# Performance work log

Measured on AMD Instinct MI355X. Metric: run time of the kernel, lower is better.

## Reference

```python
import math
import jax, jax.numpy as jnp
import numpy as np
from jax import lax

# FPN anchor layout: 1024x768 image, strides {4,8,16,32,64}, 3 anchors/location
NUM_PER_LEVEL = (147456, 36864, 9216, 2304, 576)
A_TOTAL = sum(NUM_PER_LEVEL)
BATCH = 8
PRE_NMS_TOP_N = 1000   # testing
POST_NMS_TOP_N = 1000  # testing
NMS_THRESH = 0.7
SCORE_THRESH = 0.0
MIN_SIZE = 1.0
IMG_H, IMG_W = 768.0, 1024.0
BBOX_XFORM_CLIP = math.log(1000.0 / 16.0)


def setup_inputs() -> dict:
    key = jax.random.key(0)
    k1, k2, k3, k4, k5, k6 = jax.random.split(key, 6)
    objectness = jax.random.normal(k1, (BATCH, A_TOTAL), jnp.float32)
    pred_bbox_deltas = jax.random.normal(k2, (BATCH, A_TOTAL, 4), jnp.float32) * 0.2
    # valid anchor boxes (x1, y1, x2, y2)
    cx = jax.random.uniform(k3, (A_TOTAL,), jnp.float32) * IMG_W
    cy = jax.random.uniform(k4, (A_TOTAL,), jnp.float32) * IMG_H
    w = 16.0 + jax.random.uniform(k5, (A_TOTAL,), jnp.float32) * 176.0
    h = 16.0 + jax.random.uniform(k6, (A_TOTAL,), jnp.float32) * 176.0
    anchors = jnp.stack([cx - 0.5 * w, cy - 0.5 * h, cx + 0.5 * w, cy + 0.5 * h], -1)
    return {"objectness": objectness, "pred_bbox_deltas": pred_bbox_deltas, "anchors": anchors}


def _nms_image(boxes, scores, lvl, valid):
    """batched_nms (level-offset trick) + post-NMS top-k, fixed shapes.
    boxes [K,4], scores [K], lvl [K] int, valid [K] bool -> [POST_NMS_TOP_N, 5]"""
    K = boxes.shape[0]
    s = jnp.where(valid, scores, -1.0)
    order = jnp.argsort(-s)  # decreasing score (invalid last)
    b = boxes[order]
    s = s[order]
    v = valid[order]
    # offset boxes per level so cross-level boxes never overlap (torchvision batched_nms)
    offset = lvl[order].astype(b.dtype) * (jnp.max(lax.stop_gradient(boxes)) + 1.0)
    nb = lax.stop_gradient(b) + offset[:, None]
    area = (nb[:, 2] - nb[:, 0]) * (nb[:, 3] - nb[:, 1])
    lt = jnp.maximum(nb[:, None, :2], nb[None, :, :2])  # [K,K,2]
    rb = jnp.minimum(nb[:, None, 2:], nb[None, :, 2:])
    wh = jnp.clip(rb - lt, 0.0)
    inter = wh[..., 0] * wh[..., 1]
    iou = inter / jnp.maximum(area[:, None] + area[None, :] - inter, 1e-9)
    pos = jnp.arange(K)

    def body(keep, i):
        sup = keep[i] & (iou[i] > NMS_THRESH) & (pos > i)
        return keep & ~sup, None

    keep, _ = lax.scan(body, v, pos)
    masked = jnp.where(keep, s, -1.0)
    top_s, top_i = lax.top_k(masked, POST_NMS_TOP_N)  # kept, decreasing score
    sel_b = b[top_i]
    ok = top_s > -0.5
    sel_b = jnp.where(ok[:, None], sel_b, 0.0)
    top_s = jnp.where(ok, top_s, 0.0)
    return jnp.concatenate([sel_b, top_s[:, None]], axis=-1)


def reference(objectness, pred_bbox_deltas, anchors):
    # --- box decode (BoxCoder, weights (1,1,1,1)) ---
    wa = anchors[:, 2] - anchors[:, 0]
    ha = anchors[:, 3] - anchors[:, 1]
    cxa = anchors[:, 0] + 0.5 * wa
    cya = anchors[:, 1] + 0.5 * ha
    dx, dy = pred_bbox_deltas[..., 0], pred_bbox_deltas[..., 1]
    dw = jnp.minimum(pred_bbox_deltas[..., 2], BBOX_XFORM_CLIP)
    dh = jnp.minimum(pred_bbox_deltas[..., 3], BBOX_XFORM_CLIP)
    pcx = dx * wa + cxa
    pcy = dy * ha + cya
    pw = jnp.exp(dw) * wa
    ph = jnp.exp(dh) * ha
    proposals = jnp.stack(
        [pcx - 0.5 * pw, pcy - 0.5 * ph, pcx + 0.5 * pw, pcy + 0.5 * ph], axis=-1
    )  # [B, A, 4]

    # --- per-level pre-NMS top-k (_get_top_n_idx) ---
    levels = jnp.concatenate(
        [jnp.full((n,), i, jnp.int32) for i, n in enumerate(NUM_PER_LEVEL)]
    )
    idx_parts = []
    off = 0
    for n in NUM_PER_LEVEL:
        k = min(PRE_NMS_TOP_N, n)
        _, ti = lax.top_k(objectness[:, off:off + n], k)
        idx_parts.append(ti + off)
        off += n
    top_idx = jnp.concatenate(idx_parts, axis=1)  # [B, K]

    scores = jax.nn.sigmoid(jnp.take_along_axis(objectness, top_idx, axis=1))
    lvl = levels[top_idx]
    boxes = jnp.take_along_axis(proposals, top_idx[..., None], axis=1)  # [B,K,4]

    # --- clip to image ---
    x1 = jnp.clip(boxes[..., 0], 0.0, IMG_W)
    y1 = jnp.clip(boxes[..., 1], 0.0, IMG_H)
    x2 = jnp.clip(boxes[..., 2], 0.0, IMG_W)
    y2 = jnp.clip(boxes[..., 3], 0.0, IMG_H)
    boxes = jnp.stack([x1, y1, x2, y2], axis=-1)

    # remove_small_boxes + score threshold (as validity mask; fixed shapes)
    valid = ((x2 - x1) >= MIN_SIZE) & ((y2 - y1) >= MIN_SIZE) & (scores >= SCORE_THRESH)

    # --- per-image batched NMS + post-NMS top-k ---
    return jax.vmap(_nms_image)(boxes, scores, lvl, valid)  # [B, POST_NMS_TOP_N, 5]
```

## Files before the change

### kernel.cpp

```cpp
#include <hip/hip_runtime.h>
#include <math.h>

#pragma clang fp contract(off)

#define A_TOTAL 196416
#define BATCH 8
#define KTOT 4576
#define NLEV 5
#define MSPLIT 16
#define RCAP 6144

static __device__ const int d_aoff[NLEV] = {0, 147456, 184320, 193536, 195840};
static __device__ const int d_n[NLEV]    = {147456, 36864, 9216, 2304, 576};
static __device__ const int d_k[NLEV]    = {1000, 1000, 1000, 1000, 576};
static __device__ const int d_spl[NLEV]  = {8, 2, 1, 1, 1};
static __device__ const int d_bp[NLEV]   = {0, 8, 10, 11, 12};
static __device__ const int d_pb_l[13]    = {0,0,0,0,0,0,0,0,1,1,2,3,4};
static __device__ const int d_pb_part[13] = {0,1,2,3,4,5,6,7,0,1,0,0,0};

#define TM_IOU (0.699999988079071044921875 + 0x1p-25)

__device__ inline unsigned int mono(float f) {
  unsigned int u = __float_as_uint(f);
  return (u & 0x80000000u) ? ~u : (u | 0x80000000u);
}
__device__ inline float imono(unsigned int m) {
  return __uint_as_float((m & 0x80000000u) ? (m & 0x7FFFFFFFu) : ~m);
}

__device__ inline int cnt_gt(const float* A, int n, float s) {
  int lo = 0, hi = n;
  while (lo < hi) { int mid = (lo + hi) >> 1; if (A[mid] > s) lo = mid + 1; else hi = mid; }
  return lo;
}
__device__ inline int cnt_ge(const float* A, int n, float s) {
  int lo = 0, hi = n;
  while (lo < hi) { int mid = (lo + hi) >> 1; if (A[mid] >= s) lo = mid + 1; else hi = mid; }
  return lo;
}

__global__ __launch_bounds__(1024) void k_hist(const float* __restrict__ obj,
                                               int* __restrict__ hist_g,
                                               int* __restrict__ cnt_g,
                                               float* __restrict__ maxblk) {
  int blk = blockIdx.x;
  int tid = threadIdx.x;
  if (blk == 0) {
    for (int i = tid; i < 640; i += 1024) maxblk[i] = 0.0f;
    for (int i = tid; i < 40; i += 1024) cnt_g[i] = 0;
  }
  int b = blk / 13, pb = blk % 13;
  int l = d_pb_l[pb], part = d_pb_part[pb];
  int slice = d_n[l] / d_spl[l];
  int start = d_aoff[l] + part * slice;
  const float4* p4 = (const float4*)(obj + (size_t)b * A_TOTAL + start);
  int s4 = slice >> 2;
  __shared__ int h[4096];
  for (int i = tid; i < 4096; i += 1024) h[i] = 0;
  __syncthreads();
  for (int i = tid; i < s4; i += 1024) {
    float4 v = p4[i];
    atomicAdd(&h[mono(v.x) >> 20], 1);
    atomicAdd(&h[mono(v.y) >> 20], 1);
    atomicAdd(&h[mono(v.z) >> 20], 1);
    atomicAdd(&h[mono(v.w) >> 20], 1);
  }
  __syncthreads();
  int* outp = hist_g + (size_t)blk * 4096;
  for (int i = tid; i < 4096; i += 1024) outp[i] = h[i];
}

__global__ __launch_bounds__(1024) void k_collect(const float* __restrict__ obj,
                                                  const int* __restrict__ hist_g,
                                                  int* __restrict__ cnt_g,
                                                  unsigned long long* __restrict__ cand_g) {
  int blk = blockIdx.x;
  int b = blk / 13, pb = blk % 13;
  int l = d_pb_l[pb], part = d_pb_part[pb];
  int bl = b * NLEV + l;
  const int k = d_k[l];
  int tid = threadIdx.x;
  __shared__ int t[4096];
  __shared__ int grp[256];
  __shared__ unsigned int sP;
  __shared__ __align__(16) unsigned long long lbuf[RCAP];
  __shared__ int s_cnt, s_base;
  int parts = d_spl[l];
  const int* hb = hist_g + (size_t)(b * 13 + d_bp[l]) * 4096;
  for (int bin = tid; bin < 4096; bin += 1024) {
    int s = 0;
    for (int p = 0; p < parts; ++p) s += hb[p * 4096 + bin];
    t[bin] = s;
  }
  if (tid == 0) s_cnt = 0;
  __syncthreads();
  if (tid < 256) {
    int s = 0;
    for (int j = 0; j < 16; ++j) s += t[tid * 16 + j];
    grp[tid] = s;
  }
  __syncthreads();
  if (tid == 0) {
    int cum = 0, g, d;
    for (g = 255; g >= 0; --g) {
      if (cum + grp[g] >= k) break;
      cum += grp[g];
    }
    for (d = 15; d >= 0; --d) {
      int c = t[g * 16 + d];
      if (cum + c >= k) break;
      cum += c;
    }
    sP = (unsigned int)(g * 16 + d);
  }
  __syncthreads();
  unsigned int P = sP;
  int slice = d_n[l] / parts;
  int start = d_aoff[l] + part * slice;
  const float4* p4 = (const float4*)(obj + (size_t)b * A_TOTAL + start);
  int s4 = slice >> 2;
  int lbase = part * slice;
  for (int i = tid; i < s4; i += 1024) {
    float4 v = p4[i];
    unsigned int a[4] = {mono(v.x), mono(v.y), mono(v.z), mono(v.w)};
#pragma unroll
    for (int c = 0; c < 4; ++c) {
      if ((a[c] >> 20) >= P) {
        int slot = atomicAdd(&s_cnt, 1);
        if (slot < RCAP) {
          int idx = lbase + 4 * i + c;
          lbuf[slot] = ((unsigned long long)a[c] << 32) |
                       (unsigned int)(~(unsigned int)idx);
        }
      }
    }
  }
  __syncthreads();
  int cnt = min(s_cnt, RCAP);
  if (tid == 0) s_base = atomicAdd(&cnt_g[bl], cnt);
  __syncthreads();
  int base = s_base;
  for (int i = tid; i < cnt; i += 1024) {
    int slot = base + i;
    if (slot < RCAP) cand_g[(size_t)bl * RCAP + slot] = lbuf[i];
  }
}

__global__ __launch_bounds__(256) void k_rankdec(const unsigned long long* __restrict__ cand_g,
                                                 const int* __restrict__ cnt_g,
                                                 const float* __restrict__ deltas,
                                                 const float* __restrict__ anchors,
                                                 float* __restrict__ sc0,
                                                 float4* __restrict__ box0,
                                                 float* __restrict__ maxblk) {
  int bl = blockIdx.x >> 4, part = blockIdx.x & 15;
  int b = bl / NLEV, l = bl % NLEV;
  const int k = d_k[l], aoff = d_aoff[l];
  int cnt = min(cnt_g[bl], RCAP);
  if (part * 256 >= cnt) return;
  __shared__ __align__(16) unsigned long long cb[RCAP];
  __shared__ unsigned int s_max;
  int tid = threadIdx.x;
  if (tid == 0) s_max = 0u;
  const unsigned long long* src = cand_g + (size_t)bl * RCAP;
  for (int i = tid; i < cnt; i += 256) cb[i] = src[i];
  __syncthreads();
  int myi = part * 256 + tid;
  float mx = 0.0f;
  if (myi < cnt) {
    unsigned long long e = cb[myi];
    int rank = 0;
    int nc2 = cnt >> 1;
    const ulonglong2* c2 = (const ulonglong2*)cb;
    for (int j = 0; j < nc2; ++j) {
      ulonglong2 v = c2[j];
      rank += (v.x > e) + (v.y > e);
    }
    if (cnt & 1) rank += (cb[cnt - 1] > e);
    if (rank < k) {
      unsigned int k32 = (unsigned int)(e >> 32);
      unsigned int idx = ~(unsigned int)(e & 0xFFFFFFFFull);
      float o = imono(k32);
      int gidx = aoff + (int)idx;
      const float* dl = deltas + ((size_t)b * A_TOTAL + gidx) * 4;
      const float* an = anchors + (size_t)gidx * 4;
      float a0 = an[0], a1 = an[1], a2 = an[2], a3 = an[3];
      float wa = a2 - a0, ha = a3 - a1;
      float cxa = a0 + 0.5f * wa, cya = a1 + 0.5f * ha;
      float dx = dl[0], dy = dl[1];
      const float CLIPV = 4.135166556742356f;
      float dw = fminf(dl[2], CLIPV), dh = fminf(dl[3], CLIPV);
      float pcx = dx * wa + cxa;
      float pcy = dy * ha + cya;
      float pw = (float)exp((double)dw) * wa;
      float ph = (float)exp((double)dh) * ha;
      float x1 = pcx - 0.5f * pw, y1 = pcy - 0.5f * ph;
      float x2 = pcx + 0.5f * pw, y2 = pcy + 0.5f * ph;
      x1 = fminf(fmaxf(x1, 0.0f), 1024.0f);
      x2 = fminf(fmaxf(x2, 0.0f), 1024.0f);
      y1 = fminf(fmaxf(y1, 0.0f), 768.0f);
      y2 = fminf(fmaxf(y2, 0.0f), 768.0f);
      float s = (float)(1.0 / (1.0 + exp(-(double)o)));
      bool valid = ((x2 - x1) >= 1.0f) && ((y2 - y1) >= 1.0f) && (s >= 0.0f);
      sc0[bl * 1024 + rank] = valid ? s : -1.0f;
      box0[bl * 1024 + rank] = make_float4(x1, y1, x2, y2);
      mx = fmaxf(fmaxf(x1, y1), fmaxf(x2, y2));
    }
  }
#pragma unroll
  for (int s = 1; s < 64; s <<= 1) mx = fmaxf(mx, __shfl_xor(mx, s));
  if ((tid & 63) == 0) atomicMax(&s_max, __float_as_uint(mx));
  __syncthreads();
  if (tid == 0) maxblk[blockIdx.x] = __uint_as_float(s_max);
}

__global__ __launch_bounds__(1024) void k_mask(const float* __restrict__ sc0,
                                               const float4* __restrict__ box0,
                                               const float* __restrict__ maxblk,
                                               float* __restrict__ lvlsc,
                                               float4* __restrict__ lvlraw,
                                               int* __restrict__ g_V,
                                               unsigned long long* __restrict__ masks) {
  int blk = blockIdx.x;
  int bl = blk / MSPLIT, part = blk % MSPLIT;
  int b = bl / NLEV, l = bl % NLEV;
  const int k = d_k[l];
  int tid = threadIdx.x, lane = tid & 63, w = tid >> 6;
  __shared__ float4 lbox[1024];
  __shared__ float s_mv;
  __shared__ int s_wcnt[16];
  if (w == 0) {
    float v = (lane < 80) ? maxblk[b * 80 + lane] : 0.0f;
    float v2 = (lane + 64 < 80) ? maxblk[b * 80 + lane + 64] : 0.0f;
    v = fmaxf(v, v2);
#pragma unroll
    for (int s = 1; s < 64; s <<= 1) v = fmaxf(v, __shfl_xor(v, s));
    if (lane == 0) s_mv = v;
  }
  bool in = tid < k;
  float s = in ? sc0[bl * 1024 + tid] : -1.0f;
  bool valid = in && (s >= 0.0f);
  unsigned long long mb = __ballot(valid);
  if (lane == 0) s_wcnt[w] = __popcll(mb);
  __syncthreads();
  int pre = 0;
  for (int ww = 0; ww < w; ++ww) pre += s_wcnt[ww];
  int j = pre + __popcll(mb & ((1ull << lane) - 1ull));
  int V = 0;
  for (int ww = 0; ww < 16; ++ww) V += s_wcnt[ww];
  float off = (float)l * (s_mv + 1.0f);
  if (valid) {
    float4 bx = box0[bl * 1024 + tid];
    lbox[j] = make_float4(bx.x + off, bx.y + off, bx.z + off, bx.w + off);
    if (part == 0) {
      lvlsc[bl * 1024 + j] = s;
      lvlraw[bl * 1024 + j] = bx;
    }
  }
  if (part == 0 && tid == 0) g_V[bl] = V;
  __syncthreads();
  int row0 = part * 64;
  if (row0 >= V) return;
  int i = row0 + lane;
  if (i >= V) return;
  float4 bb = lbox[i];
  float ba = (bb.z - bb.x) * (bb.w - bb.y);
  unsigned long long bits = 0ull;
  int jbase = w * 64;
  if (jbase + 63 > i && jbase < V) {
    int jhi = min(64, V - jbase);
    for (int jo = 0; jo < jhi; ++jo) {
      int jj = jbase + jo;
      float4 cb = lbox[jj];
      float ca = (cb.z - cb.x) * (cb.w - cb.y);
      float xx1 = fmaxf(bb.x, cb.x), yy1 = fmaxf(bb.y, cb.y);
      float xx2 = fminf(bb.z, cb.z), yy2 = fminf(bb.w, cb.w);
      float wd = fmaxf(xx2 - xx1, 0.0f), ht = fmaxf(yy2 - yy1, 0.0f);
      float inter = wd * ht;
      float denom = fmaxf(ba + ca - inter, 1e-9f);
      if ((jj > i) && ((double)inter >= TM_IOU * (double)denom)) bits |= (1ull << jo);
    }
  }
  masks[((size_t)bl * 16 + w) * 1024 + i] = bits;
}

__global__ __launch_bounds__(1024) void k_scan(const unsigned long long* __restrict__ masks,
                                               const int* __restrict__ g_V,
                                               unsigned long long* __restrict__ keepbits) {
  int bl = blockIdx.x;
  int tid = threadIdx.x, lane = tid & 63, w = tid >> 6;
  int V = g_V[bl];
  const int nch = (V + 63) / 64;
  const unsigned long long* M = masks + (size_t)bl * 16 * 1024;
  __shared__ unsigned long long s_remv[16];
  __shared__ unsigned long long s_D[2][72];
  __shared__ unsigned long long s_dw;
  if (tid < 16) s_remv[tid] = ~0ull;
  int base_w = w * 64;
  unsigned long long init_w;
  if (V <= base_w) init_w = ~0ull;
  else if (V >= base_w + 64) init_w = 0ull;
  else init_w = (~0ull) << (V - base_w);
  if (w == 0 && nch > 0) s_D[0][lane] = (lane < V) ? M[lane] : 0ull;
  if (tid < 8) { s_D[0][64 + tid] = 0ull; s_D[1][64 + tid] = 0ull; }
  unsigned long long acc = 0ull;
  __syncthreads();

  for (int c = 0; c < nch; ++c) {
    unsigned long long val = 0ull;
    int r = 64 * c + lane;
    if (w > c && w < nch && r < V) val = M[(size_t)w * 1024 + r];
    if (w == c) {
      unsigned long long red = acc;
#pragma unroll
      for (int s = 1; s < 64; s <<= 1) red |= __shfl_xor(red, s);
      unsigned long long dw = init_w | red;
      const unsigned long long* D = s_D[c & 1];
      unsigned long long pb[8];
#pragma unroll
      for (int u = 0; u < 8; ++u) pb[u] = D[u];
#pragma unroll
      for (int g = 0; g < 8; ++g) {
#pragma unroll
        for (int u = 0; u < 8; ++u) {
          int jj = g * 8 + u;
          if (!((dw >> jj) & 1ull)) dw |= pb[u];
          pb[u] = D[jj + 8];
        }
      }
      if (lane == 0) { s_dw = dw; s_remv[c] = dw; }
    }
    if (w == c + 1 && w < nch) {
      int rr = 64 * (c + 1) + lane;
      s_D[(c + 1) & 1][lane] = (rr < V) ? M[(size_t)(c + 1) * 1024 + rr] : 0ull;
    }
    __syncthreads();
    if (w > c && w < nch) {
      unsigned long long kept = ~s_dw;
      if ((kept >> lane) & 1ull) acc |= val;
    }
    __syncthreads();
  }
  if (tid < 16) keepbits[bl * 16 + tid] = ~s_remv[tid];
}

__global__ __launch_bounds__(1024) void k_out(const float* __restrict__ lvlsc,
                                              const float4* __restrict__ lvlraw,
                                              const unsigned long long* __restrict__ keepbits,
                                              const int* __restrict__ g_V,
                                              float* __restrict__ out) {
  int b = blockIdx.x;
  int tid = threadIdx.x, lane = tid & 63, wv = tid >> 6;
  __shared__ float ksc[NLEV * 1024];
  __shared__ int kj[NLEV * 1024];
  __shared__ int sK[NLEV];
  __shared__ int s_wcnt[16];
  for (int i = tid; i < 5000; i += 1024) out[(size_t)b * 5000 + i] = 0.0f;
  for (int l = 0; l < NLEV; ++l) {
    int bl = b * NLEV + l;
    int V = g_V[bl];
    bool kept = (tid < V) && ((keepbits[bl * 16 + (tid >> 6)] >> (tid & 63)) & 1ull);
    unsigned long long mb = __ballot(kept);
    if (lane == 0) s_wcnt[wv] = __popcll(mb);
    __syncthreads();
    int pre = 0;
    for (int w = 0; w < wv; ++w) pre += s_wcnt[w];
    int r = pre + __popcll(mb & ((1ull << lane) - 1ull));
    if (kept) { ksc[l * 1024 + r] = lvlsc[bl * 1024 + tid]; kj[l * 1024 + r] = tid; }
    if (tid == 0) {
      int t = 0;
      for (int w = 0; w < 16; ++w) t += s_wcnt[w];
      sK[l] = t;
    }
    __syncthreads();
  }
  int K[NLEV];
  for (int l = 0; l < NLEV; ++l) K[l] = sK[l];
  for (int l = 0; l < NLEV; ++l) {
    if (tid < K[l]) {
      float s = ksc[l * 1024 + tid];
      int rank = tid;
      for (int l2 = 0; l2 < NLEV; ++l2) {
        if (l2 == l) continue;
        const float* A = ksc + l2 * 1024;
        rank += (l2 < l) ? cnt_ge(A, K[l2], s) : cnt_gt(A, K[l2], s);
      }
      if (rank < 1000) {
        float4 bx = lvlraw[(size_t)(b * NLEV + l) * 1024 + kj[l * 1024 + tid]];
        float* op = out + (size_t)b * 5000 + (size_t)rank * 5;
        op[0] = bx.x; op[1] = bx.y; op[2] = bx.z; op[3] = bx.w; op[4] = s;
      }
    }
  }
}

extern "C" void kernel_launch(void* const* d_in, const int* in_sizes, int n_in,
                              void* d_out, int out_size, void* d_ws, size_t ws_size,
                              hipStream_t stream) {
  const float* obj     = (const float*)d_in[0];
  const float* deltas  = (const float*)d_in[1];
  const float* anchors = (const float*)d_in[2];
  float* out = (float*)d_out;

  char* p = (char*)d_ws;
  float4* box0   = (float4*)p; p += (size_t)40 * 1024 * sizeof(float4);
  float4* lvlraw = (float4*)p; p += (size_t)40 * 1024 * sizeof(float4);
  unsigned long long* cand_g   = (unsigned long long*)p; p += (size_t)40 * RCAP * 8;
  unsigned long long* masks    = (unsigned long long*)p; p += (size_t)40 * 16 * 1024 * 8;
  unsigned long long* keepbits = (unsigned long long*)p; p += (size_t)40 * 16 * 8;
  int*   hist_g = (int*)p;   p += (size_t)104 * 4096 * 4;
  int*   cnt_g  = (int*)p;   p += 40 * 4;
  float* maxblk = (float*)p; p += 640 * 4;
  float* sc0    = (float*)p; p += (size_t)40 * 1024 * 4;
  float* lvlsc  = (float*)p; p += (size_t)40 * 1024 * 4;
  int*   g_V    = (int*)p;   p += 40 * 4;

  hipLaunchKernelGGL(k_hist, dim3(BATCH * 13), dim3(1024), 0, stream,
                     obj, hist_g, cnt_g, maxblk);
  hipLaunchKernelGGL(k_collect, dim3(BATCH * 13), dim3(1024), 0, stream,
                     obj, hist_g, cnt_g, cand_g);
  hipLaunchKernelGGL(k_rankdec, dim3(BATCH * NLEV * 16), dim3(256), 0, stream,
                     cand_g, cnt_g, deltas, anchors, sc0, box0, maxblk);
  hipLaunchKernelGGL(k_mask, dim3(BATCH * NLEV * MSPLIT), dim3(1024), 0, stream,
                     sc0, box0, maxblk, lvlsc, lvlraw, g_V, masks);
  hipLaunchKernelGGL(k_scan, dim3(BATCH * NLEV), dim3(1024), 0, stream,
                     masks, g_V, keepbits);
  hipLaunchKernelGGL(k_out, dim3(BATCH), dim3(1024), 0, stream,
                     lvlsc, lvlraw, keepbits, g_V, out);
}
```

Before: 208.9 us.

## Fuse six NMS pipeline kernels into one cooperative kernel with grid syncs

Replaces the six separate kernel launches (histogram, collect, rank/decode, mask, scan, output) with a single cooperative kernel of 256 blocks that separates the stages with grid-wide barriers. Shared memory is pooled into one buffer reused by each stage. The rank/decode stage now uses 1024-thread tasks and reads candidates straight from global memory instead of staging them in shared memory. This removes per-launch overhead and inter-kernel gaps, but every stage is now limited to 256 resident blocks, grid.sync has its own cost, and the large shared-memory footprint may constrain occupancy.

```diff
diff --git a/kernel.cpp b/kernel.cpp
--- a/kernel.cpp
+++ b/kernel.cpp
@@ -1,14 +1,19 @@
 #include <hip/hip_runtime.h>
+#include <hip/hip_cooperative_groups.h>
 #include <math.h>
 
 #pragma clang fp contract(off)
+
+namespace cg = cooperative_groups;
+typedef unsigned long long u64;
+typedef unsigned int u32;
 
 #define A_TOTAL 196416
 #define BATCH 8
-#define KTOT 4576
 #define NLEV 5
 #define MSPLIT 16
 #define RCAP 6144
+#define NP3 (RCAP / 1024)
 
 static __device__ const int d_aoff[NLEV] = {0, 147456, 184320, 193536, 195840};
 static __device__ const int d_n[NLEV]    = {147456, 36864, 9216, 2304, 576};
@@ -20,14 +25,13 @@
 
 #define TM_IOU (0.699999988079071044921875 + 0x1p-25)
 
-__device__ inline unsigned int mono(float f) {
-  unsigned int u = __float_as_uint(f);
+__device__ inline u32 mono(float f) {
+  u32 u = __float_as_uint(f);
   return (u & 0x80000000u) ? ~u : (u | 0x80000000u);
 }
-__device__ inline float imono(unsigned int m) {
+__device__ inline float imono(u32 m) {
   return __uint_as_float((m & 0x80000000u) ? (m & 0x7FFFFFFFu) : ~m);
 }
-
 __device__ inline int cnt_gt(const float* A, int n, float s) {
   int lo = 0, hi = n;
   while (lo < hi) { int mid = (lo + hi) >> 1; if (A[mid] > s) lo = mid + 1; else hi = mid; }
@@ -39,356 +43,340 @@
   return lo;
 }
 
-__global__ __launch_bounds__(1024) void k_hist(const float* __restrict__ obj,
-                                               int* __restrict__ hist_g,
-                                               int* __restrict__ cnt_g,
-                                               float* __restrict__ maxblk) {
-  int blk = blockIdx.x;
-  int tid = threadIdx.x;
+__global__ __launch_bounds__(1024) void k_fused(
+    const float* __restrict__ obj, const float* __restrict__ deltas,
+    const float* __restrict__ anchors, float* __restrict__ out,
+    int* __restrict__ hist_g, int* __restrict__ cnt_g,
+    float* __restrict__ maxblk, u64* __restrict__ cand_g,
+    float* __restrict__ sc0, float4* __restrict__ box0,
+    float* __restrict__ lvlsc, float4* __restrict__ lvlraw,
+    int* __restrict__ g_V, u64* __restrict__ masks,
+    u64* __restrict__ keepbits) {
+  cg::grid_group grid = cg::this_grid();
+  int blk = blockIdx.x, tid = threadIdx.x, lane = tid & 63, w = tid >> 6;
+
+  __shared__ __align__(16) unsigned char smem[66560];
+  __shared__ int s_wcnt[16];
+  __shared__ int s_cnt, s_base;
+  __shared__ u32 sP, s_max;
+  __shared__ float s_mv;
+  __shared__ int sK[NLEV];
+  __shared__ u64 s_remv[16];
+  __shared__ u64 s_D[2][72];
+  __shared__ u64 s_dw;
+
   if (blk == 0) {
-    for (int i = tid; i < 640; i += 1024) maxblk[i] = 0.0f;
+    for (int i = tid; i < 240; i += 1024) maxblk[i] = 0.0f;
     for (int i = tid; i < 40; i += 1024) cnt_g[i] = 0;
   }
-  int b = blk / 13, pb = blk % 13;
-  int l = d_pb_l[pb], part = d_pb_part[pb];
-  int slice = d_n[l] / d_spl[l];
-  int start = d_aoff[l] + part * slice;
-  const float4* p4 = (const float4*)(obj + (size_t)b * A_TOTAL + start);
-  int s4 = slice >> 2;
-  __shared__ int h[4096];
-  for (int i = tid; i < 4096; i += 1024) h[i] = 0;
-  __syncthreads();
-  for (int i = tid; i < s4; i += 1024) {
-    float4 v = p4[i];
-    atomicAdd(&h[mono(v.x) >> 20], 1);
-    atomicAdd(&h[mono(v.y) >> 20], 1);
-    atomicAdd(&h[mono(v.z) >> 20], 1);
-    atomicAdd(&h[mono(v.w) >> 20], 1);
-  }
-  __syncthreads();
-  int* outp = hist_g + (size_t)blk * 4096;
-  for (int i = tid; i < 4096; i += 1024) outp[i] = h[i];
-}
-
-__global__ __launch_bounds__(1024) void k_collect(const float* __restrict__ obj,
-                                                  const int* __restrict__ hist_g,
-                                                  int* __restrict__ cnt_g,
-                                                  unsigned long long* __restrict__ cand_g) {
-  int blk = blockIdx.x;
-  int b = blk / 13, pb = blk % 13;
-  int l = d_pb_l[pb], part = d_pb_part[pb];
-  int bl = b * NLEV + l;
-  const int k = d_k[l];
-  int tid = threadIdx.x;
-  __shared__ int t[4096];
-  __shared__ int grp[256];
-  __shared__ unsigned int sP;
-  __shared__ __align__(16) unsigned long long lbuf[RCAP];
-  __shared__ int s_cnt, s_base;
-  int parts = d_spl[l];
-  const int* hb = hist_g + (size_t)(b * 13 + d_bp[l]) * 4096;
-  for (int bin = tid; bin < 4096; bin += 1024) {
-    int s = 0;
-    for (int p = 0; p < parts; ++p) s += hb[p * 4096 + bin];
-    t[bin] = s;
-  }
-  if (tid == 0) s_cnt = 0;
-  __syncthreads();
-  if (tid < 256) {
-    int s = 0;
-    for (int j = 0; j < 16; ++j) s += t[tid * 16 + j];
-    grp[tid] = s;
-  }
-  __syncthreads();
-  if (tid == 0) {
-    int cum = 0, g, d;
-    for (g = 255; g >= 0; --g) {
-      if (cum + grp[g] >= k) break;
-      cum += grp[g];
-    }
-    for (d = 15; d >= 0; --d) {
-      int c = t[g * 16 + d];
-      if (cum + c >= k) break;
-      cum += c;
-    }
-    sP = (unsigned int)(g * 16 + d);
-  }
-  __syncthreads();
-  unsigned int P = sP;
-  int slice = d_n[l] / parts;
-  int start = d_aoff[l] + part * slice;
-  const float4* p4 = (const float4*)(obj + (size_t)b * A_TOTAL + start);
-  int s4 = slice >> 2;
-  int lbase = part * slice;
-  for (int i = tid; i < s4; i += 1024) {
-    float4 v = p4[i];
-    unsigned int a[4] = {mono(v.x), mono(v.y), mono(v.z), mono(v.w)};
-#pragma unroll
-    for (int c = 0; c < 4; ++c) {
-      if ((a[c] >> 20) >= P) {
-        int slot = atomicAdd(&s_cnt, 1);
-        if (slot < RCAP) {
-          int idx = lbase + 4 * i + c;
-          lbuf[slot] = ((unsigned long long)a[c] << 32) |
-                       (unsigned int)(~(unsigned int)idx);
+  if (blk < 104) {
+    int b = blk / 13, pb = blk % 13;
+    int l = d_pb_l[pb], part = d_pb_part[pb];
+    int slice = d_n[l] / d_spl[l];
+    int start = d_aoff[l] + part * slice;
+    const float4* p4 = (const float4*)(obj + (size_t)b * A_TOTAL + start);
+    int s4 = slice >> 2;
+    int* h = (int*)smem;
+    for (int i = tid; i < 4096; i += 1024) h[i] = 0;
+    __syncthreads();
+    for (int i = tid; i < s4; i += 1024) {
+      float4 v = p4[i];
+      atomicAdd(&h[mono(v.x) >> 20], 1);
+      atomicAdd(&h[mono(v.y) >> 20], 1);
+      atomicAdd(&h[mono(v.z) >> 20], 1);
+      atomicAdd(&h[mono(v.w) >> 20], 1);
+    }
+    __syncthreads();
+    int* outp = hist_g + (size_t)blk * 4096;
+    for (int i = tid; i < 4096; i += 1024) outp[i] = h[i];
+  }
+  grid.sync();
+
+  if (blk < 104) {
+    int b = blk / 13, pb = blk % 13;
+    int l = d_pb_l[pb], part = d_pb_part[pb];
+    int bl = b * NLEV + l;
+    const int k = d_k[l];
+    int* t = (int*)smem;
+    int* grp = (int*)(smem + 16384);
+    u64* lbuf = (u64*)(smem + 17408);
+    int parts = d_spl[l];
+    const int* hb = hist_g + (size_t)(b * 13 + d_bp[l]) * 4096;
+    for (int bin = tid; bin < 4096; bin += 1024) {
+      int s = 0;
+      for (int p = 0; p < parts; ++p) s += hb[p * 4096 + bin];
+      t[bin] = s;
+    }
+    if (tid == 0) s_cnt = 0;
+    __syncthreads();
+    if (tid < 256) {
+      int s = 0;
+      for (int j = 0; j < 16; ++j) s += t[tid * 16 + j];
+      grp[tid] = s;
+    }
+    __syncthreads();
+    if (tid == 0) {
+      int cum = 0, g, d;
+      for (g = 255; g >= 0; --g) {
+        if (cum + grp[g] >= k) break;
+        cum += grp[g];
+      }
+      for (d = 15; d >= 0; --d) {
+        int c = t[g * 16 + d];
+        if (cum + c >= k) break;
+        cum += c;
+      }
+      sP = (u32)(g * 16 + d);
+    }
+    __syncthreads();
+    u32 P = sP;
+    int slice = d_n[l] / parts;
+    int start = d_aoff[l] + part * slice;
+    const float4* p4 = (const float4*)(obj + (size_t)b * A_TOTAL + start);
+    int s4 = slice >> 2;
+    int lbase = part * slice;
+    for (int i = tid; i < s4; i += 1024) {
+      float4 v = p4[i];
+      u32 a[4] = {mono(v.x), mono(v.y), mono(v.z), mono(v.w)};
+#pragma unroll
+      for (int c = 0; c < 4; ++c) {
+        if ((a[c] >> 20) >= P) {
+          int slot = atomicAdd(&s_cnt, 1);
+          if (slot < RCAP) {
+            int idx = lbase + 4 * i + c;
+            lbuf[slot] = ((u64)a[c] << 32) | (u32)(~(u32)idx);
+          }
         }
       }
     }
-  }
-  __syncthreads();
-  int cnt = min(s_cnt, RCAP);
-  if (tid == 0) s_base = atomicAdd(&cnt_g[bl], cnt);
-  __syncthreads();
-  int base = s_base;
-  for (int i = tid; i < cnt; i += 1024) {
-    int slot = base + i;
-    if (slot < RCAP) cand_g[(size_t)bl * RCAP + slot] = lbuf[i];
-  }
-}
-
-__global__ __launch_bounds__(256) void k_rankdec(const unsigned long long* __restrict__ cand_g,
-                                                 const int* __restrict__ cnt_g,
-                                                 const float* __restrict__ deltas,
-                                                 const float* __restrict__ anchors,
-                                                 float* __restrict__ sc0,
-                                                 float4* __restrict__ box0,
-                                                 float* __restrict__ maxblk) {
-  int bl = blockIdx.x >> 4, part = blockIdx.x & 15;
-  int b = bl / NLEV, l = bl % NLEV;
-  const int k = d_k[l], aoff = d_aoff[l];
-  int cnt = min(cnt_g[bl], RCAP);
-  if (part * 256 >= cnt) return;
-  __shared__ __align__(16) unsigned long long cb[RCAP];
-  __shared__ unsigned int s_max;
-  int tid = threadIdx.x;
-  if (tid == 0) s_max = 0u;
-  const unsigned long long* src = cand_g + (size_t)bl * RCAP;
-  for (int i = tid; i < cnt; i += 256) cb[i] = src[i];
-  __syncthreads();
-  int myi = part * 256 + tid;
-  float mx = 0.0f;
-  if (myi < cnt) {
-    unsigned long long e = cb[myi];
-    int rank = 0;
-    int nc2 = cnt >> 1;
-    const ulonglong2* c2 = (const ulonglong2*)cb;
-    for (int j = 0; j < nc2; ++j) {
-      ulonglong2 v = c2[j];
-      rank += (v.x > e) + (v.y > e);
-    }
-    if (cnt & 1) rank += (cb[cnt - 1] > e);
-    if (rank < k) {
-      unsigned int k32 = (unsigned int)(e >> 32);
-      unsigned int idx = ~(unsigned int)(e & 0xFFFFFFFFull);
-      float o = imono(k32);
-      int gidx = aoff + (int)idx;
-      const float* dl = deltas + ((size_t)b * A_TOTAL + gidx) * 4;
-      const float* an = anchors + (size_t)gidx * 4;
-      float a0 = an[0], a1 = an[1], a2 = an[2], a3 = an[3];
-      float wa = a2 - a0, ha = a3 - a1;
-      float cxa = a0 + 0.5f * wa, cya = a1 + 0.5f * ha;
-      float dx = dl[0], dy = dl[1];
-      const float CLIPV = 4.135166556742356f;
-      float dw = fminf(dl[2], CLIPV), dh = fminf(dl[3], CLIPV);
-      float pcx = dx * wa + cxa;
-      float pcy = dy * ha + cya;
-      float pw = (float)exp((double)dw) * wa;
-      float ph = (float)exp((double)dh) * ha;
-      float x1 = pcx - 0.5f * pw, y1 = pcy - 0.5f * ph;
-      float x2 = pcx + 0.5f * pw, y2 = pcy + 0.5f * ph;
-      x1 = fminf(fmaxf(x1, 0.0f), 1024.0f);
-      x2 = fminf(fmaxf(x2, 0.0f), 1024.0f);
-      y1 = fminf(fmaxf(y1, 0.0f), 768.0f);
-      y2 = fminf(fmaxf(y2, 0.0f), 768.0f);
-      float s = (float)(1.0 / (1.0 + exp(-(double)o)));
-      bool valid = ((x2 - x1) >= 1.0f) && ((y2 - y1) >= 1.0f) && (s >= 0.0f);
-      sc0[bl * 1024 + rank] = valid ? s : -1.0f;
-      box0[bl * 1024 + rank] = make_float4(x1, y1, x2, y2);
-      mx = fmaxf(fmaxf(x1, y1), fmaxf(x2, y2));
-    }
-  }
-#pragma unroll
-  for (int s = 1; s < 64; s <<= 1) mx = fmaxf(mx, __shfl_xor(mx, s));
-  if ((tid & 63) == 0) atomicMax(&s_max, __float_as_uint(mx));
-  __syncthreads();
-  if (tid == 0) maxblk[blockIdx.x] = __uint_as_float(s_max);
-}
-
-__global__ __launch_bounds__(1024) void k_mask(const float* __restrict__ sc0,
-                                               const float4* __restrict__ box0,
-                                               const float* __restrict__ maxblk,
-                                               float* __restrict__ lvlsc,
-                                               float4* __restrict__ lvlraw,
-                                               int* __restrict__ g_V,
-                                               unsigned long long* __restrict__ masks) {
-  int blk = blockIdx.x;
-  int bl = blk / MSPLIT, part = blk % MSPLIT;
-  int b = bl / NLEV, l = bl % NLEV;
-  const int k = d_k[l];
-  int tid = threadIdx.x, lane = tid & 63, w = tid >> 6;
-  __shared__ float4 lbox[1024];
-  __shared__ float s_mv;
-  __shared__ int s_wcnt[16];
-  if (w == 0) {
-    float v = (lane < 80) ? maxblk[b * 80 + lane] : 0.0f;
-    float v2 = (lane + 64 < 80) ? maxblk[b * 80 + lane + 64] : 0.0f;
-    v = fmaxf(v, v2);
-#pragma unroll
-    for (int s = 1; s < 64; s <<= 1) v = fmaxf(v, __shfl_xor(v, s));
-    if (lane == 0) s_mv = v;
-  }
-  bool in = tid < k;
-  float s = in ? sc0[bl * 1024 + tid] : -1.0f;
-  bool valid = in && (s >= 0.0f);
-  unsigned long long mb = __ballot(valid);
-  if (lane == 0) s_wcnt[w] = __popcll(mb);
-  __syncthreads();
-  int pre = 0;
-  for (int ww = 0; ww < w; ++ww) pre += s_wcnt[ww];
-  int j = pre + __popcll(mb & ((1ull << lane) - 1ull));
-  int V = 0;
-  for (int ww = 0; ww < 16; ++ww) V += s_wcnt[ww];
-  float off = (float)l * (s_mv + 1.0f);
-  if (valid) {
-    float4 bx = box0[bl * 1024 + tid];
-    lbox[j] = make_float4(bx.x + off, bx.y + off, bx.z + off, bx.w + off);
-    if (part == 0) {
-      lvlsc[bl * 1024 + j] = s;
-      lvlraw[bl * 1024 + j] = bx;
-    }
-  }
-  if (part == 0 && tid == 0) g_V[bl] = V;
-  __syncthreads();
-  int row0 = part * 64;
-  if (row0 >= V) return;
-  int i = row0 + lane;
-  if (i >= V) return;
-  float4 bb = lbox[i];
-  float ba = (bb.z - bb.x) * (bb.w - bb.y);
-  unsigned long long bits = 0ull;
-  int jbase = w * 64;
-  if (jbase + 63 > i && jbase < V) {
-    int jhi = min(64, V - jbase);
-    for (int jo = 0; jo < jhi; ++jo) {
-      int jj = jbase + jo;
-      float4 cb = lbox[jj];
-      float ca = (cb.z - cb.x) * (cb.w - cb.y);
-      float xx1 = fmaxf(bb.x, cb.x), yy1 = fmaxf(bb.y, cb.y);
-      float xx2 = fminf(bb.z, cb.z), yy2 = fminf(bb.w, cb.w);
-      float wd = fmaxf(xx2 - xx1, 0.0f), ht = fmaxf(yy2 - yy1, 0.0f);
-      float inter = wd * ht;
-      float denom = fmaxf(ba + ca - inter, 1e-9f);
-      if ((jj > i) && ((double)inter >= TM_IOU * (double)denom)) bits |= (1ull << jo);
-    }
-  }
-  masks[((size_t)bl * 16 + w) * 1024 + i] = bits;
-}
-
-__global__ __launch_bounds__(1024) void k_scan(const unsigned long long* __restrict__ masks,
-                                               const int* __restrict__ g_V,
-                                               unsigned long long* __restrict__ keepbits) {
-  int bl = blockIdx.x;
-  int tid = threadIdx.x, lane = tid & 63, w = tid >> 6;
-  int V = g_V[bl];
-  const int nch = (V + 63) / 64;
-  const unsigned long long* M = masks + (size_t)bl * 16 * 1024;
-  __shared__ unsigned long long s_remv[16];
-  __shared__ unsigned long long s_D[2][72];
-  __shared__ unsigned long long s_dw;
-  if (tid < 16) s_remv[tid] = ~0ull;
-  int base_w = w * 64;
-  unsigned long long init_w;
-  if (V <= base_w) init_w = ~0ull;
-  else if (V >= base_w + 64) init_w = 0ull;
-  else init_w = (~0ull) << (V - base_w);
-  if (w == 0 && nch > 0) s_D[0][lane] = (lane < V) ? M[lane] : 0ull;
-  if (tid < 8) { s_D[0][64 + tid] = 0ull; s_D[1][64 + tid] = 0ull; }
-  unsigned long long acc = 0ull;
-  __syncthreads();
-
-  for (int c = 0; c < nch; ++c) {
-    unsigned long long val = 0ull;
-    int r = 64 * c + lane;
-    if (w > c && w < nch && r < V) val = M[(size_t)w * 1024 + r];
-    if (w == c) {
-      unsigned long long red = acc;
-#pragma unroll
-      for (int s = 1; s < 64; s <<= 1) red |= __shfl_xor(red, s);
-      unsigned long long dw = init_w | red;
-      const unsigned long long* D = s_D[c & 1];
-      unsigned long long pb[8];
-#pragma unroll
-      for (int u = 0; u < 8; ++u) pb[u] = D[u];
-#pragma unroll
-      for (int g = 0; g < 8; ++g) {
-#pragma unroll
-        for (int u = 0; u < 8; ++u) {
-          int jj = g * 8 + u;
-          if (!((dw >> jj) & 1ull)) dw |= pb[u];
-          pb[u] = D[jj + 8];
+    __syncthreads();
+    int cnt = min(s_cnt, RCAP);
+    if (tid == 0) s_base = atomicAdd(&cnt_g[bl], cnt);
+    __syncthreads();
+    int base = s_base;
+    for (int i = tid; i < cnt; i += 1024) {
+      int slot = base + i;
+      if (slot < RCAP) cand_g[(size_t)bl * RCAP + slot] = lbuf[i];
+    }
+  }
+  grid.sync();
+
+  for (int task = blk; task < 40 * NP3; task += 256) {
+    int bl = task / NP3, part = task % NP3;
+    int cnt = min(cnt_g[bl], RCAP);
+    if (part * 1024 >= cnt) continue;
+    int b = bl / NLEV, l = bl % NLEV;
+    const int k = d_k[l], aoff = d_aoff[l];
+    const u64* src = cand_g + (size_t)bl * RCAP;
+    if (tid == 0) s_max = 0u;
+    __syncthreads();
+    int myi = part * 1024 + tid;
+    float mx = 0.0f;
+    if (myi < cnt) {
+      u64 e = src[myi];
+      int rank = 0;
+      const ulonglong2* c2 = (const ulonglong2*)src;
+      int nc2 = cnt >> 1;
+#pragma unroll 4
+      for (int j = 0; j < nc2; ++j) {
+        ulonglong2 v = c2[j];
+        rank += (v.x > e) + (v.y > e);
+      }
+      if (cnt & 1) rank += (src[cnt - 1] > e);
+      if (rank < k) {
+        u32 k32 = (u32)(e >> 32);
+        u32 idx = ~(u32)(e & 0xFFFFFFFFull);
+        float o = imono(k32);
+        int gidx = aoff + (int)idx;
+        const float* dl = deltas + ((size_t)b * A_TOTAL + gidx) * 4;
+        const float* an = anchors + (size_t)gidx * 4;
+        float a0 = an[0], a1 = an[1], a2 = an[2], a3 = an[3];
+        float wa = a2 - a0, ha = a3 - a1;
+        float cxa = a0 + 0.5f * wa, cya = a1 + 0.5f * ha;
+        float dx = dl[0], dy = dl[1];
+        const float CLIPV = 4.135166556742356f;
+        float dw = fminf(dl[2], CLIPV), dh = fminf(dl[3], CLIPV);
+        float pcx = dx * wa + cxa;
+        float pcy = dy * ha + cya;
+        float pw = (float)exp((double)dw) * wa;
+        float ph = (float)exp((double)dh) * ha;
+        float x1 = pcx - 0.5f * pw, y1 = pcy - 0.5f * ph;
+        float x2 = pcx + 0.5f * pw, y2 = pcy + 0.5f * ph;
+        x1 = fminf(fmaxf(x1, 0.0f), 1024.0f);
+        x2 = fminf(fmaxf(x2, 0.0f), 1024.0f);
+        y1 = fminf(fmaxf(y1, 0.0f), 768.0f);
+        y2 = fminf(fmaxf(y2, 0.0f), 768.0f);
+        float s = (float)(1.0 / (1.0 + exp(-(double)o)));
+        bool valid = ((x2 - x1) >= 1.0f) && ((y2 - y1) >= 1.0f) && (s >= 0.0f);
+        sc0[bl * 1024 + rank] = valid ? s : -1.0f;
+        box0[bl * 1024 + rank] = make_float4(x1, y1, x2, y2);
+        mx = fmaxf(fmaxf(x1, y1), fmaxf(x2, y2));
+      }
+    }
+#pragma unroll
+    for (int s = 1; s < 64; s <<= 1) mx = fmaxf(mx, __shfl_xor(mx, s));
+    if (lane == 0) atomicMax(&s_max, __float_as_uint(mx));
+    __syncthreads();
+    if (tid == 0) maxblk[task] = __uint_as_float(s_max);
+    __syncthreads();
+  }
+  grid.sync();
+
+  for (int task = blk; task < 40 * MSPLIT; task += 256) {
+    int bl = task >> 4, part = task & 15;
+    int b = bl / NLEV, l = bl % NLEV;
+    const int k = d_k[l];
+    float4* lbox = (float4*)smem;
+    if (w == 0) {
+      float v = (lane < 30) ? maxblk[b * 30 + lane] : 0.0f;
+#pragma unroll
+      for (int s = 1; s < 64; s <<= 1) v = fmaxf(v, __shfl_xor(v, s));
+      if (lane == 0) s_mv = v;
+    }
+    bool in = tid < k;
+    float s = in ? sc0[bl * 1024 + tid] : -1.0f;
+    bool valid = in && (s >= 0.0f);
+    u64 mb = __ballot(valid);
+    if (lane == 0) s_wcnt[w] = __popcll(mb);
+    __syncthreads();
+    int pre = 0;
+    for (int ww = 0; ww < w; ++ww) pre += s_wcnt[ww];
+    int j = pre + __popcll(mb & ((1ull << lane) - 1ull));
+    int V = 0;
+    for (int ww = 0; ww < 16; ++ww) V += s_wcnt[ww];
+    float off = (float)l * (s_mv + 1.0f);
+    if (valid) {
+      float4 bx = box0[bl * 1024 + tid];
+      lbox[j] = make_float4(bx.x + off, bx.y + off, bx.z + off, bx.w + off);
+      if (part == 0) {
+        lvlsc[bl * 1024 + j] = s;
+        lvlraw[bl * 1024 + j] = bx;
+      }
+    }
+    if (part == 0 && tid == 0) g_V[bl] = V;
+    __syncthreads();
+    int row0 = part * 64;
+    if (row0 < V) {
+      int i = row0 + lane;
+      if (i < V) {
+        float4 bb = lbox[i];
+        float ba = (bb.z - bb.x) * (bb.w - bb.y);
+        u64 bits = 0ull;
+        int jbase = w * 64;
+        if (jbase + 63 > i && jbase < V) {
+          int jhi = min(64, V - jbase);
+          for (int jo = 0; jo < jhi; ++jo) {
+            int jj = jbase + jo;
+            float4 cb = lbox[jj];
+            float ca = (cb.z - cb.x) * (cb.w - cb.y);
+            float xx1 = fmaxf(bb.x, cb.x), yy1 = fmaxf(bb.y, cb.y);
+            float xx2 = fminf(bb.z, cb.z), yy2 = fminf(bb.w, cb.w);
+            float wd = fmaxf(xx2 - xx1, 0.0f), ht = fmaxf(yy2 - yy1, 0.0f);
+            float inter = wd * ht;
+            float denom = fmaxf(ba + ca - inter, 1e-9f);
+            if ((jj > i) && ((double)inter >= TM_IOU * (double)denom)) bits |= (1ull << jo);
+          }
         }
-      }
-      if (lane == 0) { s_dw = dw; s_remv[c] = dw; }
-    }
-    if (w == c + 1 && w < nch) {
-      int rr = 64 * (c + 1) + lane;
-      s_D[(c + 1) & 1][lane] = (rr < V) ? M[(size_t)(c + 1) * 1024 + rr] : 0ull;
-    }
-    __syncthreads();
-    if (w > c && w < nch) {
-      unsigned long long kept = ~s_dw;
-      if ((kept >> lane) & 1ull) acc |= val;
-    }
-    __syncthreads();
-  }
-  if (tid < 16) keepbits[bl * 16 + tid] = ~s_remv[tid];
-}
-
-__global__ __launch_bounds__(1024) void k_out(const float* __restrict__ lvlsc,
-                                              const float4* __restrict__ lvlraw,
-                                              const unsigned long long* __restrict__ keepbits,
-                                              const int* __restrict__ g_V,
-                                              float* __restrict__ out) {
-  int b = blockIdx.x;
-  int tid = threadIdx.x, lane = tid & 63, wv = tid >> 6;
-  __shared__ float ksc[NLEV * 1024];
-  __shared__ int kj[NLEV * 1024];
-  __shared__ int sK[NLEV];
-  __shared__ int s_wcnt[16];
-  for (int i = tid; i < 5000; i += 1024) out[(size_t)b * 5000 + i] = 0.0f;
-  for (int l = 0; l < NLEV; ++l) {
-    int bl = b * NLEV + l;
+        masks[((size_t)bl * 16 + w) * 1024 + i] = bits;
+      }
+    }
+    __syncthreads();
+  }
+  grid.sync();
+
+  if (blk < 40) {
+    int bl = blk;
     int V = g_V[bl];
-    bool kept = (tid < V) && ((keepbits[bl * 16 + (tid >> 6)] >> (tid & 63)) & 1ull);
-    unsigned long long mb = __ballot(kept);
-    if (lane == 0) s_wcnt[wv] = __popcll(mb);
-    __syncthreads();
-    int pre = 0;
-    for (int w = 0; w < wv; ++w) pre += s_wcnt[w];
-    int r = pre + __popcll(mb & ((1ull << lane) - 1ull));
-    if (kept) { ksc[l * 1024 + r] = lvlsc[bl * 1024 + tid]; kj[l * 1024 + r] = tid; }
-    if (tid == 0) {
-      int t = 0;
-      for (int w = 0; w < 16; ++w) t += s_wcnt[w];
-      sK[l] = t;
-    }
-    __syncthreads();
-  }
-  int K[NLEV];
-  for (int l = 0; l < NLEV; ++l) K[l] = sK[l];
-  for (int l = 0; l < NLEV; ++l) {
-    if (tid < K[l]) {
-      float s = ksc[l * 1024 + tid];
-      int rank = tid;
-      for (int l2 = 0; l2 < NLEV; ++l2) {
-        if (l2 == l) continue;
-        const float* A = ksc + l2 * 1024;
-        rank += (l2 < l) ? cnt_ge(A, K[l2], s) : cnt_gt(A, K[l2], s);
-      }
-      if (rank < 1000) {
-        float4 bx = lvlraw[(size_t)(b * NLEV + l) * 1024 + kj[l * 1024 + tid]];
-        float* op = out + (size_t)b * 5000 + (size_t)rank * 5;
-        op[0] = bx.x; op[1] = bx.y; op[2] = bx.z; op[3] = bx.w; op[4] = s;
+    const int nch = (V + 63) / 64;
+    const u64* M = masks + (size_t)bl * 16 * 1024;
+    if (tid < 16) s_remv[tid] = ~0ull;
+    int base_w = w * 64;
+    u64 init_w;
+    if (V <= base_w) init_w = ~0ull;
+    else if (V >= base_w + 64) init_w = 0ull;
+    else init_w = (~0ull) << (V - base_w);
+    if (w == 0 && nch > 0) s_D[0][lane] = (lane < V) ? M[lane] : 0ull;
+    if (tid < 8) { s_D[0][64 + tid] = 0ull; s_D[1][64 + tid] = 0ull; }
+    u64 acc = 0ull;
+    __syncthreads();
+    for (int c = 0; c < nch; ++c) {
+      u64 val = 0ull;
+      int r = 64 * c + lane;
+      if (w > c && w < nch && r < V) val = M[(size_t)w * 1024 + r];
+      if (w == c) {
+        u64 red = acc;
+#pragma unroll
+        for (int s = 1; s < 64; s <<= 1) red |= __shfl_xor(red, s);
+        u64 dw = init_w | red;
+        const u64* D = s_D[c & 1];
+        u64 pb[8];
+#pragma unroll
+        for (int u = 0; u < 8; ++u) pb[u] = D[u];
+#pragma unroll
+        for (int g = 0; g < 8; ++g) {
+#pragma unroll
+          for (int u = 0; u < 8; ++u) {
+            int jj = g * 8 + u;
+            if (!((dw >> jj) & 1ull)) dw |= pb[u];
+            pb[u] = D[jj + 8];
+          }
+        }
+        if (lane == 0) { s_dw = dw; s_remv[c] = dw; }
+      }
+      if (w == c + 1 && w < nch) {
+        int rr = 64 * (c + 1) + lane;
+        s_D[(c + 1) & 1][lane] = (rr < V) ? M[(size_t)(c + 1) * 1024 + rr] : 0ull;
+      }
+      __syncthreads();
+      if (w > c && w < nch) {
+        u64 kept = ~s_dw;
+        if ((kept >> lane) & 1ull) acc |= val;
+      }
+      __syncthreads();
+    }
+    if (tid < 16) keepbits[bl * 16 + tid] = ~s_remv[tid];
+  }
+  grid.sync();
+
+  if (blk < 8) {
+    int b = blk;
+    float* ksc = (float*)smem;
+    int* kj = (int*)(smem + 20480);
+    for (int i = tid; i < 5000; i += 1024) out[(size_t)b * 5000 + i] = 0.0f;
+    for (int l = 0; l < NLEV; ++l) {
+      int bl = b * NLEV + l;
+      int V = g_V[bl];
+      bool kept = (tid < V) && ((keepbits[bl * 16 + (tid >> 6)] >> (tid & 63)) & 1ull);
+      u64 mb = __ballot(kept);
+      if (lane == 0) s_wcnt[w] = __popcll(mb);
+      __syncthreads();
+      int pre = 0;
+      for (int ww = 0; ww < w; ++ww) pre += s_wcnt[ww];
+      int r = pre + __popcll(mb & ((1ull << lane) - 1ull));
+      if (kept) { ksc[l * 1024 + r] = lvlsc[bl * 1024 + tid]; kj[l * 1024 + r] = tid; }
+      if (tid == 0) {
+        int t = 0;
+        for (int ww = 0; ww < 16; ++ww) t += s_wcnt[ww];
+        sK[l] = t;
+      }
+      __syncthreads();
+    }
+    int K[NLEV];
+    for (int l = 0; l < NLEV; ++l) K[l] = sK[l];
+    for (int l = 0; l < NLEV; ++l) {
+      if (tid < K[l]) {
+        float s = ksc[l * 1024 + tid];
+        int rank = tid;
+        for (int l2 = 0; l2 < NLEV; ++l2) {
+          if (l2 == l) continue;
+          const float* A = ksc + l2 * 1024;
+          rank += (l2 < l) ? cnt_ge(A, K[l2], s) : cnt_gt(A, K[l2], s);
+        }
+        if (rank < 1000) {
+          float4 bx = lvlraw[(size_t)(b * NLEV + l) * 1024 + kj[l * 1024 + tid]];
+          float* op = out + (size_t)b * 5000 + (size_t)rank * 5;
+          op[0] = bx.x; op[1] = bx.y; op[2] = bx.z; op[3] = bx.w; op[4] = s;
+        }
       }
     }
   }
@@ -405,26 +393,17 @@
   char* p = (char*)d_ws;
   float4* box0   = (float4*)p; p += (size_t)40 * 1024 * sizeof(float4);
   float4* lvlraw = (float4*)p; p += (size_t)40 * 1024 * sizeof(float4);
-  unsigned long long* cand_g   = (unsigned long long*)p; p += (size_t)40 * RCAP * 8;
-  unsigned long long* masks    = (unsigned long long*)p; p += (size_t)40 * 16 * 1024 * 8;
-  unsigned long long* keepbits = (unsigned long long*)p; p += (size_t)40 * 16 * 8;
+  u64* cand_g   = (u64*)p; p += (size_t)40 * RCAP * 8;
+  u64* masks    = (u64*)p; p += (size_t)40 * 16 * 1024 * 8;
+  u64* keepbits = (u64*)p; p += (size_t)40 * 16 * 8;
   int*   hist_g = (int*)p;   p += (size_t)104 * 4096 * 4;
   int*   cnt_g  = (int*)p;   p += 40 * 4;
-  float* maxblk = (float*)p; p += 640 * 4;
+  float* maxblk = (float*)p; p += 256 * 4;
   float* sc0    = (float*)p; p += (size_t)40 * 1024 * 4;
   float* lvlsc  = (float*)p; p += (size_t)40 * 1024 * 4;
   int*   g_V    = (int*)p;   p += 40 * 4;
 
-  hipLaunchKernelGGL(k_hist, dim3(BATCH * 13), dim3(1024), 0, stream,
-                     obj, hist_g, cnt_g, maxblk);
-  hipLaunchKernelGGL(k_collect, dim3(BATCH * 13), dim3(1024), 0, stream,
-                     obj, hist_g, cnt_g, cand_g);
-  hipLaunchKernelGGL(k_rankdec, dim3(BATCH * NLEV * 16), dim3(256), 0, stream,
-                     cand_g, cnt_g, deltas, anchors, sc0, box0, maxblk);
-  hipLaunchKernelGGL(k_mask, dim3(BATCH * NLEV * MSPLIT), dim3(1024), 0, stream,
-                     sc0, box0, maxblk, lvlsc, lvlraw, g_V, masks);
-  hipLaunchKernelGGL(k_scan, dim3(BATCH * NLEV), dim3(1024), 0, stream,
-                     masks, g_V, keepbits);
-  hipLaunchKernelGGL(k_out, dim3(BATCH), dim3(1024), 0, stream,
-                     lvlsc, lvlraw, keepbits, g_V, out);
-}
+  void* args[] = {&obj, &deltas, &anchors, &out, &hist_g, &cnt_g, &maxblk,
+                  &cand_g, &sc0, &box0, &lvlsc, &lvlraw, &g_V, &masks, &keepbits};
+  hipLaunchCooperativeKernel((void*)k_fused, dim3(256), dim3(1024), args, 0, stream);
+}
```

New measurement: 394.2 us. 1.89x slower.
